# Kernel tuning notes

Hardware: AMD Instinct MI355X
Metric: run time of the kernel (lower is better)

## Reference

```python
import jax, jax.numpy as jnp
import numpy as np

B, S, D = 2, 2048, 2048
H, G = 16, 4
HD = D // H          # head_dim = 128
KV = HD * G          # 512


def setup_inputs() -> dict:
    key = jax.random.key(0)
    ks = jax.random.split(key, 5)
    scale = 1.0 / np.sqrt(D)
    return {
        "x": jax.random.normal(ks[0], (B, S, D), dtype=jnp.float32),
        "Wqkv": jax.random.normal(ks[1], (D, D + 2 * KV), dtype=jnp.float32) * scale,
        "bqkv": jax.random.normal(ks[2], (D + 2 * KV,), dtype=jnp.float32) * 0.01,
        "Wout": jax.random.normal(ks[3], (D, D), dtype=jnp.float32) * scale,
        "bout": jax.random.normal(ks[4], (D,), dtype=jnp.float32) * 0.01,
    }


def reference(x, Wqkv, bqkv, Wout, bout):
    b, s, _ = x.shape
    qkv = x @ Wqkv + bqkv                                  # [b, s, D + 2*KV]
    q, k, v = jnp.split(qkv, [D, D + KV], axis=-1)
    q = q.reshape(b, s, H, HD)                             # [b, s, H, hd]
    # torch .repeat tiles the group axis: head h -> group (h % G)
    k = jnp.tile(k.reshape(b, s, G, HD), (1, 1, H // G, 1))  # [b, s, H, hd]
    v = jnp.tile(v.reshape(b, s, G, HD), (1, 1, H // G, 1))
    # NOTE: original divides by head_dim (not sqrt(head_dim)) -- kept faithfully
    scores = jnp.einsum("bqhd,bkhd->bhqk", q, k) / HD      # [b, H, s, s]
    prob = jax.nn.softmax(scores, axis=-1)
    out = jnp.einsum("bhqk,bkhd->bqhd", prob, v).reshape(b, s, D)
    return out @ Wout + bout
```

## Files before the change

kernel.cpp:

```cpp
#include <hip/hip_runtime.h>
#include <stdint.h>

typedef __bf16 bf16;
typedef __bf16 bf16x8 __attribute__((ext_vector_type(8)));
typedef __bf16 bf16x4 __attribute__((ext_vector_type(4)));
typedef float  f32x4  __attribute__((ext_vector_type(4)));

#define B_   2
#define S_   2048
#define D_   2048
#define H_   16
#define G_   4
#define HD_  128
#define KV_  512
#define NQKV 3072
#define M_   4096

__device__ __forceinline__ void async16(bf16* lds, const bf16* g) {
  __builtin_amdgcn_global_load_lds(
      (const __attribute__((address_space(1))) unsigned int*)g,
      (__attribute__((address_space(3))) unsigned int*)lds, 16, 0, 0);
}

__device__ __forceinline__ f32x4 mfma16(bf16x8 a, bf16x8 b, f32x4 c) {
  return __builtin_amdgcn_mfma_f32_16x16x32_bf16(a, b, c, 0, 0, 0);
}

__global__ void convert_x_kernel(const float* __restrict__ in,
                                 bf16* __restrict__ out, int n4) {
  int i = blockIdx.x * blockDim.x + threadIdx.x;
  if (i >= n4) return;
  float4 v = ((const float4*)in)[i];
  bf16x4 o = { (bf16)v.x, (bf16)v.y, (bf16)v.z, (bf16)v.w };
  *(bf16x4*)(out + (size_t)i * 4) = o;
}

__global__ void transpose_w_kernel(const float* __restrict__ in,
                                   bf16* __restrict__ out,
                                   int rows, int cols) {
  __shared__ float tile[32][33];
  int bc = blockIdx.x * 32;
  int br = blockIdx.y * 32;
  int tx = threadIdx.x, ty = threadIdx.y;
  #pragma unroll
  for (int i = 0; i < 32; i += 8)
    tile[ty + i][tx] = in[(size_t)(br + ty + i) * cols + bc + tx];
  __syncthreads();
  #pragma unroll
  for (int i = 0; i < 32; i += 8)
    out[(size_t)(bc + ty + i) * rows + br + tx] = (bf16)tile[tx][ty + i];
}

__global__ void transpose_v_kernel(const bf16* __restrict__ qkv,
                                   bf16* __restrict__ vt) {
  __shared__ bf16 tile[32][33];
  int bg = blockIdx.z; int b = bg / G_, g = bg % G_;
  int sb = blockIdx.x * 32, db = blockIdx.y * 32;
  int tx = threadIdx.x, ty = threadIdx.y;
  const bf16* src = qkv + (size_t)b * S_ * NQKV + (D_ + KV_ + g * HD_);
  #pragma unroll
  for (int i = 0; i < 32; i += 8)
    tile[ty + i][tx] = src[(size_t)(sb + ty + i) * NQKV + db + tx];
  __syncthreads();
  bf16* dst = vt + (size_t)(b * G_ + g) * HD_ * S_;
  #pragma unroll
  for (int i = 0; i < 32; i += 8)
    dst[(size_t)(db + ty + i) * S_ + sb + tx] = tile[tx][ty + i];
}

template <int OUT_BF16>
__global__ __launch_bounds__(256) void gemm_bt(const bf16* __restrict__ A,
                                               const bf16* __restrict__ Bt,
                                               const float* __restrict__ bias,
                                               void* __restrict__ Cout,
                                               int Ndim, int K) {
  __shared__ __align__(16) bf16 As[128 * 32];
  __shared__ __align__(16) bf16 Bs[128 * 32];
  int t = threadIdx.x;
  int w = t >> 6, l = t & 63, lr = l & 15, lg = l >> 4;
  int wm = w >> 1, wn = w & 1;
  int row0 = blockIdx.x * 128, col0 = blockIdx.y * 128;

  f32x4 acc[4][4] = {};

  const bf16* ga = A  + (size_t)(row0 + (t >> 2)) * K + (t & 3) * 8;
  const bf16* gb = Bt + (size_t)(col0 + (t >> 2)) * K + (t & 3) * 8;

  for (int k0 = 0; k0 < K; k0 += 32) {
    __syncthreads();
    #pragma unroll
    for (int i = 0; i < 2; i++)
      async16(&As[w * 512 + i * 2048], ga + (size_t)i * 64 * K + k0);
    #pragma unroll
    for (int i = 0; i < 2; i++)
      async16(&Bs[w * 512 + i * 2048], gb + (size_t)i * 64 * K + k0);
    __syncthreads();

    bf16x8 af[4], bfr[4];
    #pragma unroll
    for (int mi = 0; mi < 4; mi++)
      af[mi] = *(const bf16x8*)&As[(wm * 64 + mi * 16 + lr) * 32 + lg * 8];
    #pragma unroll
    for (int ni = 0; ni < 4; ni++)
      bfr[ni] = *(const bf16x8*)&Bs[(wn * 64 + ni * 16 + lr) * 32 + lg * 8];
    #pragma unroll
    for (int mi = 0; mi < 4; mi++)
      #pragma unroll
      for (int ni = 0; ni < 4; ni++)
        acc[mi][ni] = mfma16(af[mi], bfr[ni], acc[mi][ni]);
  }

  float bv[4];
  #pragma unroll
  for (int ni = 0; ni < 4; ni++)
    bv[ni] = bias[col0 + wn * 64 + ni * 16 + lr];

  #pragma unroll
  for (int mi = 0; mi < 4; mi++)
    #pragma unroll
    for (int ni = 0; ni < 4; ni++)
      #pragma unroll
      for (int r = 0; r < 4; r++) {
        int row = row0 + wm * 64 + mi * 16 + lg * 4 + r;
        int col = col0 + wn * 64 + ni * 16 + lr;
        float v = acc[mi][ni][r] + bv[ni];
        if (OUT_BF16)
          ((bf16*)Cout)[(size_t)row * Ndim + col] = (bf16)v;
        else
          ((float*)Cout)[(size_t)row * Ndim + col] = v;
      }
}

__global__ __launch_bounds__(256, 2) void attn_kernel(const bf16* __restrict__ qkv,
                                                      const bf16* __restrict__ vt,
                                                      bf16* __restrict__ attnb) {
  __shared__ __align__(16) bf16 Ks[2][64 * 128];
  __shared__ __align__(16) bf16 Vs[2][128 * 64];
  __shared__ __align__(16) bf16 Ps[4][32 * 64];

  int t = threadIdx.x, w = t >> 6, l = t & 63, lr = l & 15, lg = l >> 4;
  int rsw = lr & 7;
  int lin = blockIdx.x + gridDim.x * blockIdx.y;
  int swz = (lin & 7) * 64 + (lin >> 3);
  int q0 = (swz & 15) * 128;
  int bh = swz >> 4, b = bh >> 4, h = bh & 15, g = h & 3;

  bf16x8 qf[2][4];
  #pragma unroll
  for (int mi = 0; mi < 2; mi++) {
    const bf16* qbase = qkv + (size_t)(b * S_ + q0 + w * 32 + mi * 16 + lr) * NQKV + h * HD_;
    #pragma unroll
    for (int kc = 0; kc < 4; kc++)
      qf[mi][kc] = *(const bf16x8*)(qbase + kc * 32 + lg * 8);
  }

  const bf16* kbase = qkv + (size_t)b * S_ * NQKV + D_ + g * HD_;
  const bf16* vbase = vt + (size_t)(b * G_ + g) * HD_ * S_;

  int krowi = w * 4 + (l >> 4);
  int ksw = (l & 15) ^ (krowi & 7);
  const bf16* kgl = kbase + (size_t)krowi * NQKV + ksw * 8;
  int vrowi = w * 8 + (l >> 3);
  int vsw = (l & 7) ^ ((l >> 3) & 7);
  const bf16* vgl = vbase + (size_t)vrowi * S_ + vsw * 8;

  auto STAGE_KV = [&](int nb, int kv0) {
    #pragma unroll
    for (int i = 0; i < 4; i++)
      async16(&Ks[nb][w * 512 + i * 2048], kgl + (size_t)(kv0 + i * 16) * NQKV);
    #pragma unroll
    for (int i = 0; i < 4; i++)
      async16(&Vs[nb][w * 512 + i * 2048], vgl + (size_t)(i * 32) * S_ + kv0);
  };

  float lsump[2] = {};
  f32x4 accO[2][8] = {};

  STAGE_KV(0, 0);

  for (int ti = 0; ti < S_ / 64; ++ti) {
    int cur = ti & 1;
    __syncthreads();
    if (ti + 1 < S_ / 64) STAGE_KV(cur ^ 1, (ti + 1) * 64);

    const bf16* ks = &Ks[cur][0];
    const bf16* vs = &Vs[cur][0];

    f32x4 sacc[2][4] = {};
    __builtin_amdgcn_s_setprio(1);
    #pragma unroll
    for (int fk = 0; fk < 4; fk++) {
      bf16x8 kf[4];
      #pragma unroll
      for (int kc = 0; kc < 4; kc++)
        kf[kc] = *(const bf16x8*)&ks[(fk * 16 + lr) * 128 + (((kc * 4 + lg) ^ rsw) * 8)];
      #pragma unroll
      for (int mi = 0; mi < 2; mi++)
        #pragma unroll
        for (int kc = 0; kc < 4; kc++)
          sacc[mi][fk] = mfma16(kf[kc], qf[mi][kc], sacc[mi][fk]);
    }
    __builtin_amdgcn_s_setprio(0);

    bf16* psw = &Ps[w][0];
    #pragma unroll
    for (int mi = 0; mi < 2; mi++)
      #pragma unroll
      for (int fk = 0; fk < 4; fk++) {
        float p0 = __expf(sacc[mi][fk][0] * 0.0078125f);
        float p1 = __expf(sacc[mi][fk][1] * 0.0078125f);
        float p2 = __expf(sacc[mi][fk][2] * 0.0078125f);
        float p3 = __expf(sacc[mi][fk][3] * 0.0078125f);
        lsump[mi] += (p0 + p1) + (p2 + p3);
        bf16x4 pk = { (bf16)p0, (bf16)p1, (bf16)p2, (bf16)p3 };
        *(bf16x4*)&psw[(mi * 16 + lr) * 64 +
                       (((fk * 2 + (lg >> 1)) ^ rsw) * 8) + (lg & 1) * 4] = pk;
      }

    bf16x8 pa[2][2];
    #pragma unroll
    for (int mi = 0; mi < 2; mi++)
      #pragma unroll
      for (int kk = 0; kk < 2; kk++)
        pa[mi][kk] = *(const bf16x8*)&psw[(mi * 16 + lr) * 64 + (((kk * 4 + lg) ^ rsw) * 8)];

    __builtin_amdgcn_s_setprio(1);
    #pragma unroll
    for (int fd = 0; fd < 8; fd++) {
      bf16x8 vfr[2];
      #pragma unroll
      for (int kk = 0; kk < 2; kk++)
        vfr[kk] = *(const bf16x8*)&vs[(fd * 16 + lr) * 64 + (((kk * 4 + lg) ^ rsw) * 8)];
      #pragma unroll
      for (int mi = 0; mi < 2; mi++)
        #pragma unroll
        for (int kk = 0; kk < 2; kk++)
          accO[mi][fd] = mfma16(pa[mi][kk], vfr[kk], accO[mi][fd]);
    }
    __builtin_amdgcn_s_setprio(0);
  }

  #pragma unroll
  for (int mi = 0; mi < 2; mi++) {
    float s = lsump[mi];
    s += __shfl_xor(s, 16);
    s += __shfl_xor(s, 32);
    float rls[4];
    #pragma unroll
    for (int r = 0; r < 4; r++) rls[r] = 1.f / __shfl(s, lg * 4 + r);
    bf16* obase = attnb + (size_t)(b * S_ + q0 + w * 32 + mi * 16) * D_ + h * HD_;
    #pragma unroll
    for (int r = 0; r < 4; r++)
      #pragma unroll
      for (int fd = 0; fd < 8; fd++)
        obase[(size_t)(lg * 4 + r) * D_ + fd * 16 + lr] =
            (bf16)(accO[mi][fd][r] * rls[r]);
  }
}

extern "C" void kernel_launch(void* const* d_in, const int* in_sizes, int n_in,
                              void* d_out, int out_size, void* d_ws, size_t ws_size,
                              hipStream_t stream) {
  const float* x    = (const float*)d_in[0];
  const float* Wqkv = (const float*)d_in[1];
  const float* bqkv = (const float*)d_in[2];
  const float* Wout = (const float*)d_in[3];
  const float* bout = (const float*)d_in[4];
  float* out = (float*)d_out;

  char* p = (char*)d_ws;
  bf16* xb    = (bf16*)p; p += (size_t)M_ * D_ * 2;
  bf16* wqkvT = (bf16*)p; p += (size_t)NQKV * D_ * 2;
  bf16* woutT = (bf16*)p; p += (size_t)D_ * D_ * 2;
  bf16* qkvb  = (bf16*)p; p += (size_t)M_ * NQKV * 2;
  bf16* vtb   = (bf16*)p; p += (size_t)B_ * G_ * HD_ * S_ * 2;
  bf16* attnb = (bf16*)p; p += (size_t)M_ * D_ * 2;

  convert_x_kernel<<<dim3(M_ * D_ / 4 / 256), dim3(256), 0, stream>>>(x, xb, M_ * D_ / 4);
  transpose_w_kernel<<<dim3(NQKV / 32, D_ / 32), dim3(32, 8), 0, stream>>>(Wqkv, wqkvT, D_, NQKV);
  transpose_w_kernel<<<dim3(D_ / 32, D_ / 32), dim3(32, 8), 0, stream>>>(Wout, woutT, D_, D_);

  gemm_bt<1><<<dim3(M_ / 128, NQKV / 128), dim3(256), 0, stream>>>(xb, wqkvT, bqkv, (void*)qkvb, NQKV, D_);

  transpose_v_kernel<<<dim3(S_ / 32, HD_ / 32, B_ * G_), dim3(32, 8), 0, stream>>>(qkvb, vtb);

  attn_kernel<<<dim3(S_ / 128, B_ * H_), dim3(256), 0, stream>>>(qkvb, vtb, attnb);

  gemm_bt<0><<<dim3(M_ / 128, D_ / 128), dim3(256), 0, stream>>>(attnb, woutT, bout, (void*)out, D_, D_);
}
```

Baseline: 220.1 us.

## Load V fragments directly from global into registers, drop V LDS staging

Removes the V tile from shared memory and loads each wave's V fragments straight from the transposed V buffer in global memory into registers, software-pipelined against the PV MFMAs. It also fuses the exp/softmax step into each QK^T fk chunk so the full sacc array no longer has to be live at once. Launch bounds are raised to 3 waves per SIMD to use the freed LDS and registers. The cost is that V reads now go through global/L2 with per-wave redundancy and exposed latency instead of one shared async copy per block.

```diff
diff --git a/kernel.cpp b/kernel.cpp
--- a/kernel.cpp
+++ b/kernel.cpp
@@ -131,11 +131,10 @@
       }
 }
 
-__global__ __launch_bounds__(256, 2) void attn_kernel(const bf16* __restrict__ qkv,
+__global__ __launch_bounds__(256, 3) void attn_kernel(const bf16* __restrict__ qkv,
                                                       const bf16* __restrict__ vt,
                                                       bf16* __restrict__ attnb) {
   __shared__ __align__(16) bf16 Ks[2][64 * 128];
-  __shared__ __align__(16) bf16 Vs[2][128 * 64];
   __shared__ __align__(16) bf16 Ps[4][32 * 64];
 
   int t = threadIdx.x, w = t >> 6, l = t & 63, lr = l & 15, lg = l >> 4;
@@ -160,33 +159,49 @@
   int krowi = w * 4 + (l >> 4);
   int ksw = (l & 15) ^ (krowi & 7);
   const bf16* kgl = kbase + (size_t)krowi * NQKV + ksw * 8;
-  int vrowi = w * 8 + (l >> 3);
-  int vsw = (l & 7) ^ ((l >> 3) & 7);
-  const bf16* vgl = vbase + (size_t)vrowi * S_ + vsw * 8;
-
-  auto STAGE_KV = [&](int nb, int kv0) {
+  const bf16* vg = vbase + (size_t)lr * S_ + lg * 8;
+
+  auto STAGE_K = [&](int nb, int kv0) {
     #pragma unroll
     for (int i = 0; i < 4; i++)
       async16(&Ks[nb][w * 512 + i * 2048], kgl + (size_t)(kv0 + i * 16) * NQKV);
-    #pragma unroll
-    for (int i = 0; i < 4; i++)
-      async16(&Vs[nb][w * 512 + i * 2048], vgl + (size_t)(i * 32) * S_ + kv0);
   };
+
+#define LOADV(dst, p)                                                         \
+    _Pragma("unroll")                                                         \
+    for (int fd2 = 0; fd2 < 2; fd2++)                                         \
+      _Pragma("unroll")                                                       \
+      for (int kk = 0; kk < 2; kk++)                                          \
+        dst[fd2][kk] = *(const bf16x8*)(vg + (size_t)((p) * 32 + fd2 * 16) * S_ \
+                                        + kv0 + kk * 32);
+
+#define PVQ(p, V)                                                             \
+    _Pragma("unroll")                                                         \
+    for (int fd2 = 0; fd2 < 2; fd2++)                                         \
+      _Pragma("unroll")                                                       \
+      for (int mi = 0; mi < 2; mi++)                                          \
+        _Pragma("unroll")                                                     \
+        for (int kk = 0; kk < 2; kk++)                                        \
+          accO[mi][(p) * 2 + fd2] =                                           \
+              mfma16(pa[mi][kk], V[fd2][kk], accO[mi][(p) * 2 + fd2]);
 
   float lsump[2] = {};
   f32x4 accO[2][8] = {};
 
-  STAGE_KV(0, 0);
+  STAGE_K(0, 0);
 
   for (int ti = 0; ti < S_ / 64; ++ti) {
     int cur = ti & 1;
+    int kv0 = ti * 64;
     __syncthreads();
-    if (ti + 1 < S_ / 64) STAGE_KV(cur ^ 1, (ti + 1) * 64);
+    if (ti + 1 < S_ / 64) STAGE_K(cur ^ 1, kv0 + 64);
+
+    bf16x8 vr0[2][2], vr1[2][2];
+    LOADV(vr0, 0);
 
     const bf16* ks = &Ks[cur][0];
-    const bf16* vs = &Vs[cur][0];
-
-    f32x4 sacc[2][4] = {};
+    bf16* psw = &Ps[w][0];
+
     __builtin_amdgcn_s_setprio(1);
     #pragma unroll
     for (int fk = 0; fk < 4; fk++) {
@@ -194,28 +209,25 @@
       #pragma unroll
       for (int kc = 0; kc < 4; kc++)
         kf[kc] = *(const bf16x8*)&ks[(fk * 16 + lr) * 128 + (((kc * 4 + lg) ^ rsw) * 8)];
+      f32x4 sacc[2] = {};
       #pragma unroll
       for (int mi = 0; mi < 2; mi++)
         #pragma unroll
         for (int kc = 0; kc < 4; kc++)
-          sacc[mi][fk] = mfma16(kf[kc], qf[mi][kc], sacc[mi][fk]);
-    }
-    __builtin_amdgcn_s_setprio(0);
-
-    bf16* psw = &Ps[w][0];
-    #pragma unroll
-    for (int mi = 0; mi < 2; mi++)
-      #pragma unroll
-      for (int fk = 0; fk < 4; fk++) {
-        float p0 = __expf(sacc[mi][fk][0] * 0.0078125f);
-        float p1 = __expf(sacc[mi][fk][1] * 0.0078125f);
-        float p2 = __expf(sacc[mi][fk][2] * 0.0078125f);
-        float p3 = __expf(sacc[mi][fk][3] * 0.0078125f);
+          sacc[mi] = mfma16(kf[kc], qf[mi][kc], sacc[mi]);
+      #pragma unroll
+      for (int mi = 0; mi < 2; mi++) {
+        float p0 = __expf(sacc[mi][0] * 0.0078125f);
+        float p1 = __expf(sacc[mi][1] * 0.0078125f);
+        float p2 = __expf(sacc[mi][2] * 0.0078125f);
+        float p3 = __expf(sacc[mi][3] * 0.0078125f);
         lsump[mi] += (p0 + p1) + (p2 + p3);
         bf16x4 pk = { (bf16)p0, (bf16)p1, (bf16)p2, (bf16)p3 };
         *(bf16x4*)&psw[(mi * 16 + lr) * 64 +
                        (((fk * 2 + (lg >> 1)) ^ rsw) * 8) + (lg & 1) * 4] = pk;
       }
+    }
+    __builtin_amdgcn_s_setprio(0);
 
     bf16x8 pa[2][2];
     #pragma unroll
@@ -225,18 +237,13 @@
         pa[mi][kk] = *(const bf16x8*)&psw[(mi * 16 + lr) * 64 + (((kk * 4 + lg) ^ rsw) * 8)];
 
     __builtin_amdgcn_s_setprio(1);
-    #pragma unroll
-    for (int fd = 0; fd < 8; fd++) {
-      bf16x8 vfr[2];
-      #pragma unroll
-      for (int kk = 0; kk < 2; kk++)
-        vfr[kk] = *(const bf16x8*)&vs[(fd * 16 + lr) * 64 + (((kk * 4 + lg) ^ rsw) * 8)];
-      #pragma unroll
-      for (int mi = 0; mi < 2; mi++)
-        #pragma unroll
-        for (int kk = 0; kk < 2; kk++)
-          accO[mi][fd] = mfma16(pa[mi][kk], vfr[kk], accO[mi][fd]);
-    }
+    LOADV(vr1, 1);
+    PVQ(0, vr0);
+    LOADV(vr0, 2);
+    PVQ(1, vr1);
+    LOADV(vr1, 3);
+    PVQ(2, vr0);
+    PVQ(3, vr1);
     __builtin_amdgcn_s_setprio(0);
   }
 
@@ -256,6 +263,8 @@
         obase[(size_t)(lg * 4 + r) * D_ + fd * 16 + lr] =
             (bf16)(accO[mi][fd][r] * rls[r]);
   }
+#undef LOADV
+#undef PVQ
 }
 
 extern "C" void kernel_launch(void* const* d_in, const int* in_sizes, int n_in,
```

After: 365.8 us. 1.66x slower.

## Halve attention KV tile to 32 and raise occupancy to three blocks per CU

Applied to the files above, without the earlier changes.

Shrinks the per-iteration K/V tile from 64 to 32 keys, halving the LDS footprint of the K, V and P buffers, and raises launch bounds to allow three workgroups per CU. The softmax exponentials are now computed right after each 16-key score fragment, so fewer score accumulators are live at once. The swizzle patterns are adjusted for the narrower tiles. In exchange the loop runs twice as many iterations, each with its own barrier and async staging, so synchronisation overhead grows and there is less MFMA work per barrier to hide latency.

```diff
diff --git a/kernel.cpp b/kernel.cpp
--- a/kernel.cpp
+++ b/kernel.cpp
@@ -131,12 +131,12 @@
       }
 }
 
-__global__ __launch_bounds__(256, 2) void attn_kernel(const bf16* __restrict__ qkv,
+__global__ __launch_bounds__(256, 3) void attn_kernel(const bf16* __restrict__ qkv,
                                                       const bf16* __restrict__ vt,
                                                       bf16* __restrict__ attnb) {
-  __shared__ __align__(16) bf16 Ks[2][64 * 128];
-  __shared__ __align__(16) bf16 Vs[2][128 * 64];
-  __shared__ __align__(16) bf16 Ps[4][32 * 64];
+  __shared__ __align__(16) bf16 Ks[2][32 * 128];
+  __shared__ __align__(16) bf16 Vs[2][128 * 32];
+  __shared__ __align__(16) bf16 Ps[4][32 * 32];
 
   int t = threadIdx.x, w = t >> 6, l = t & 63, lr = l & 15, lg = l >> 4;
   int rsw = lr & 7;
@@ -160,17 +160,17 @@
   int krowi = w * 4 + (l >> 4);
   int ksw = (l & 15) ^ (krowi & 7);
   const bf16* kgl = kbase + (size_t)krowi * NQKV + ksw * 8;
-  int vrowi = w * 8 + (l >> 3);
-  int vsw = (l & 7) ^ ((l >> 3) & 7);
+  int vrowi = w * 16 + (l >> 2);
+  int vsw = (l & 3) ^ (vrowi & 3);
   const bf16* vgl = vbase + (size_t)vrowi * S_ + vsw * 8;
 
   auto STAGE_KV = [&](int nb, int kv0) {
     #pragma unroll
-    for (int i = 0; i < 4; i++)
-      async16(&Ks[nb][w * 512 + i * 2048], kgl + (size_t)(kv0 + i * 16) * NQKV);
-    #pragma unroll
-    for (int i = 0; i < 4; i++)
-      async16(&Vs[nb][w * 512 + i * 2048], vgl + (size_t)(i * 32) * S_ + kv0);
+    for (int i = 0; i < 2; i++)
+      async16(&Ks[nb][i * 2048 + w * 512], kgl + (size_t)(kv0 + i * 16) * NQKV);
+    #pragma unroll
+    for (int i = 0; i < 2; i++)
+      async16(&Vs[nb][i * 2048 + w * 512], vgl + (size_t)(i * 64) * S_ + kv0);
   };
 
   float lsump[2] = {};
@@ -178,64 +178,55 @@
 
   STAGE_KV(0, 0);
 
-  for (int ti = 0; ti < S_ / 64; ++ti) {
+  for (int ti = 0; ti < S_ / 32; ++ti) {
     int cur = ti & 1;
+    int kv0 = ti * 32;
     __syncthreads();
-    if (ti + 1 < S_ / 64) STAGE_KV(cur ^ 1, (ti + 1) * 64);
+    if (ti + 1 < S_ / 32) STAGE_KV(cur ^ 1, kv0 + 32);
 
     const bf16* ks = &Ks[cur][0];
     const bf16* vs = &Vs[cur][0];
-
-    f32x4 sacc[2][4] = {};
+    bf16* psw = &Ps[w][0];
+
     __builtin_amdgcn_s_setprio(1);
     #pragma unroll
-    for (int fk = 0; fk < 4; fk++) {
+    for (int fk = 0; fk < 2; fk++) {
       bf16x8 kf[4];
       #pragma unroll
       for (int kc = 0; kc < 4; kc++)
         kf[kc] = *(const bf16x8*)&ks[(fk * 16 + lr) * 128 + (((kc * 4 + lg) ^ rsw) * 8)];
+      f32x4 sacc[2] = {};
       #pragma unroll
       for (int mi = 0; mi < 2; mi++)
         #pragma unroll
         for (int kc = 0; kc < 4; kc++)
-          sacc[mi][fk] = mfma16(kf[kc], qf[mi][kc], sacc[mi][fk]);
+          sacc[mi] = mfma16(kf[kc], qf[mi][kc], sacc[mi]);
+      #pragma unroll
+      for (int mi = 0; mi < 2; mi++) {
+        float p0 = __expf(sacc[mi][0] * 0.0078125f);
+        float p1 = __expf(sacc[mi][1] * 0.0078125f);
+        float p2 = __expf(sacc[mi][2] * 0.0078125f);
+        float p3 = __expf(sacc[mi][3] * 0.0078125f);
+        lsump[mi] += (p0 + p1) + (p2 + p3);
+        bf16x4 pk = { (bf16)p0, (bf16)p1, (bf16)p2, (bf16)p3 };
+        *(bf16x4*)&psw[(mi * 16 + lr) * 32 +
+                       (((fk * 2 + (lg >> 1)) ^ (lr & 3)) * 8) + (lg & 1) * 4] = pk;
+      }
     }
     __builtin_amdgcn_s_setprio(0);
 
-    bf16* psw = &Ps[w][0];
+    bf16x8 pa[2];
     #pragma unroll
     for (int mi = 0; mi < 2; mi++)
-      #pragma unroll
-      for (int fk = 0; fk < 4; fk++) {
-        float p0 = __expf(sacc[mi][fk][0] * 0.0078125f);
-        float p1 = __expf(sacc[mi][fk][1] * 0.0078125f);
-        float p2 = __expf(sacc[mi][fk][2] * 0.0078125f);
-        float p3 = __expf(sacc[mi][fk][3] * 0.0078125f);
-        lsump[mi] += (p0 + p1) + (p2 + p3);
-        bf16x4 pk = { (bf16)p0, (bf16)p1, (bf16)p2, (bf16)p3 };
-        *(bf16x4*)&psw[(mi * 16 + lr) * 64 +
-                       (((fk * 2 + (lg >> 1)) ^ rsw) * 8) + (lg & 1) * 4] = pk;
-      }
-
-    bf16x8 pa[2][2];
-    #pragma unroll
-    for (int mi = 0; mi < 2; mi++)
-      #pragma unroll
-      for (int kk = 0; kk < 2; kk++)
-        pa[mi][kk] = *(const bf16x8*)&psw[(mi * 16 + lr) * 64 + (((kk * 4 + lg) ^ rsw) * 8)];
+      pa[mi] = *(const bf16x8*)&psw[(mi * 16 + lr) * 32 + ((lg ^ (lr & 3)) * 8)];
 
     __builtin_amdgcn_s_setprio(1);
     #pragma unroll
     for (int fd = 0; fd < 8; fd++) {
-      bf16x8 vfr[2];
-      #pragma unroll
-      for (int kk = 0; kk < 2; kk++)
-        vfr[kk] = *(const bf16x8*)&vs[(fd * 16 + lr) * 64 + (((kk * 4 + lg) ^ rsw) * 8)];
+      bf16x8 vfr = *(const bf16x8*)&vs[(fd * 16 + lr) * 32 + ((lg ^ (lr & 3)) * 8)];
       #pragma unroll
       for (int mi = 0; mi < 2; mi++)
-        #pragma unroll
-        for (int kk = 0; kk < 2; kk++)
-          accO[mi][fd] = mfma16(pa[mi][kk], vfr[kk], accO[mi][fd]);
+        accO[mi][fd] = mfma16(pa[mi], vfr, accO[mi][fd]);
     }
     __builtin_amdgcn_s_setprio(0);
   }
```

Measured after the change: 237.6 us. +8.0%, slower.

## Add 256x256 eight-wave phased GEMM for QKV projection and interleave softmax in attention

Applied to the files above, without the earlier changes.

Adds a new GEMM kernel with 256x256 tiles, 512 threads, and four-phase staggered async loads to LDS, each phase overlapping one slice of the next tile's loads with MFMA work. It replaces the 128x128 GEMM used for the QKV projection. Larger tiles cut global traffic per FLOP, at the cost of more registers and LDS and only 192 blocks in the grid. The attention kernel also computes exp and writes P to LDS per key fragment right after its score MFMAs, which shortens score-register lifetimes and interleaves VALU with MFMA work.

```diff
diff --git a/kernel.cpp b/kernel.cpp
--- a/kernel.cpp
+++ b/kernel.cpp
@@ -131,6 +131,128 @@
       }
 }
 
+template <int OUT_BF16>
+__global__ __launch_bounds__(512, 2) void gemm_8ph(const bf16* __restrict__ A,
+                                                   const bf16* __restrict__ Bt,
+                                                   const float* __restrict__ bias,
+                                                   void* __restrict__ Cout,
+                                                   int Ndim, int K, int nbm) {
+  __shared__ __align__(16) bf16 Ash[2][2][128 * 64];
+  __shared__ __align__(16) bf16 Bsh[2][2][128 * 64];
+
+  int t = threadIdx.x, w = t >> 6, l = t & 63, lr = l & 15, lg = l >> 4;
+  int wm = w >> 2, wn = w & 3;
+  int rsw = lr & 7;
+  int brow0 = (wn & 1) * 64;
+  int bh_ = wn >> 1;
+
+  int cpx = (int)gridDim.x >> 3;
+  int swz = ((int)blockIdx.x & 7) * cpx + ((int)blockIdx.x >> 3);
+  int row0 = (swz % nbm) * 256, col0 = (swz / nbm) * 256;
+
+  int r_ = t >> 3;
+  int csw = (t & 7) ^ (r_ & 7);
+  const bf16* gA = A  + (size_t)(row0 + r_) * K + csw * 8;
+  const bf16* gB = Bt + (size_t)(col0 + r_) * K + csw * 8;
+  int dofs = r_ * 64 + (t & 7) * 8;
+
+  const int NT = K >> 6;
+  f32x4 acc[8][4] = {};
+
+  auto stage2 = [&](int b, int kt, int p) {
+    size_t ko = (size_t)kt * 64;
+    if (p == 0) {
+      async16(&Bsh[b][0][dofs],        gB + ko);
+      async16(&Bsh[b][0][dofs + 4096], gB + (size_t)64 * K + ko);
+    } else if (p == 1) {
+      async16(&Bsh[b][1][dofs],        gB + (size_t)128 * K + ko);
+      async16(&Bsh[b][1][dofs + 4096], gB + (size_t)192 * K + ko);
+    } else if (p == 2) {
+      async16(&Ash[b][0][dofs],        gA + ko);
+      async16(&Ash[b][1][dofs],        gA + (size_t)128 * K + ko);
+    } else {
+      async16(&Ash[b][0][dofs + 4096], gA + (size_t)64 * K + ko);
+      async16(&Ash[b][1][dofs + 4096], gA + (size_t)192 * K + ko);
+    }
+  };
+
+#define LDA8(mi, kc) (*(const bf16x8*)&asb[((mi) * 16 + lr) * 64 + ((((kc) * 4 + lg) ^ rsw) * 8)])
+#define LDB8(ni, kc) (*(const bf16x8*)&bsb[(brow0 + (ni) * 16 + lr) * 64 + ((((kc) * 4 + lg) ^ rsw) * 8)])
+#define PHASE(q) { \
+    bf16x8 a00 = LDA8(2*(q), 0),   a01 = LDA8(2*(q), 1); \
+    bf16x8 a10 = LDA8(2*(q)+1, 0), a11 = LDA8(2*(q)+1, 1); \
+    __builtin_amdgcn_s_setprio(1); \
+    _Pragma("unroll") \
+    for (int ni = 0; ni < 4; ni++) { \
+      acc[2*(q)][ni]   = mfma16(a00, bfr[ni][0], acc[2*(q)][ni]); \
+      acc[2*(q)][ni]   = mfma16(a01, bfr[ni][1], acc[2*(q)][ni]); \
+      acc[2*(q)+1][ni] = mfma16(a10, bfr[ni][0], acc[2*(q)+1][ni]); \
+      acc[2*(q)+1][ni] = mfma16(a11, bfr[ni][1], acc[2*(q)+1][ni]); \
+    } \
+    __builtin_amdgcn_s_setprio(0); }
+
+  stage2(0, 0, 0); stage2(0, 0, 1); stage2(0, 0, 2); stage2(0, 0, 3);
+
+  for (int kt = 0; kt < NT; ++kt) {
+    int bc = kt & 1;
+    int nlast = (kt + 1 < NT);
+    asm volatile("s_waitcnt vmcnt(2)" ::: "memory");
+    __builtin_amdgcn_sched_barrier(0);
+    __builtin_amdgcn_s_barrier();
+
+    const bf16* asb = &Ash[bc][wm][0];
+    const bf16* bsb = &Bsh[bc][bh_][0];
+
+    bf16x8 bfr[4][2];
+    #pragma unroll
+    for (int ni = 0; ni < 4; ni++) {
+      bfr[ni][0] = LDB8(ni, 0);
+      bfr[ni][1] = LDB8(ni, 1);
+    }
+    if (nlast) stage2(bc ^ 1, kt + 1, 0);
+    PHASE(0);
+    __builtin_amdgcn_s_barrier();
+
+    if (nlast) stage2(bc ^ 1, kt + 1, 1);
+    PHASE(1);
+
+    if (nlast) { asm volatile("s_waitcnt vmcnt(4)" ::: "memory"); }
+    else       { asm volatile("s_waitcnt vmcnt(0)" ::: "memory"); }
+    __builtin_amdgcn_sched_barrier(0);
+    __builtin_amdgcn_s_barrier();
+
+    if (nlast) stage2(bc ^ 1, kt + 1, 2);
+    PHASE(2);
+    __builtin_amdgcn_s_barrier();
+
+    if (nlast) stage2(bc ^ 1, kt + 1, 3);
+    PHASE(3);
+  }
+
+  float bv[4];
+  #pragma unroll
+  for (int ni = 0; ni < 4; ni++)
+    bv[ni] = bias[col0 + wn * 64 + ni * 16 + lr];
+
+  #pragma unroll
+  for (int mi = 0; mi < 8; mi++)
+    #pragma unroll
+    for (int ni = 0; ni < 4; ni++)
+      #pragma unroll
+      for (int r = 0; r < 4; r++) {
+        int row = row0 + wm * 128 + mi * 16 + lg * 4 + r;
+        int col = col0 + wn * 64 + ni * 16 + lr;
+        float v = acc[mi][ni][r] + bv[ni];
+        if (OUT_BF16)
+          ((bf16*)Cout)[(size_t)row * Ndim + col] = (bf16)v;
+        else
+          ((float*)Cout)[(size_t)row * Ndim + col] = v;
+      }
+#undef LDA8
+#undef LDB8
+#undef PHASE
+}
+
 __global__ __launch_bounds__(256, 2) void attn_kernel(const bf16* __restrict__ qkv,
                                                       const bf16* __restrict__ vt,
                                                       bf16* __restrict__ attnb) {
@@ -180,13 +302,14 @@
 
   for (int ti = 0; ti < S_ / 64; ++ti) {
     int cur = ti & 1;
+    int kv0 = ti * 64;
     __syncthreads();
-    if (ti + 1 < S_ / 64) STAGE_KV(cur ^ 1, (ti + 1) * 64);
+    if (ti + 1 < S_ / 64) STAGE_KV(cur ^ 1, kv0 + 64);
 
     const bf16* ks = &Ks[cur][0];
     const bf16* vs = &Vs[cur][0];
-
-    f32x4 sacc[2][4] = {};
+    bf16* psw = &Ps[w][0];
+
     __builtin_amdgcn_s_setprio(1);
     #pragma unroll
     for (int fk = 0; fk < 4; fk++) {
@@ -194,28 +317,25 @@
       #pragma unroll
       for (int kc = 0; kc < 4; kc++)
         kf[kc] = *(const bf16x8*)&ks[(fk * 16 + lr) * 128 + (((kc * 4 + lg) ^ rsw) * 8)];
+      f32x4 sacc[2] = {};
       #pragma unroll
       for (int mi = 0; mi < 2; mi++)
         #pragma unroll
         for (int kc = 0; kc < 4; kc++)
-          sacc[mi][fk] = mfma16(kf[kc], qf[mi][kc], sacc[mi][fk]);
-    }
-    __builtin_amdgcn_s_setprio(0);
-
-    bf16* psw = &Ps[w][0];
-    #pragma unroll
-    for (int mi = 0; mi < 2; mi++)
-      #pragma unroll
-      for (int fk = 0; fk < 4; fk++) {
-        float p0 = __expf(sacc[mi][fk][0] * 0.0078125f);
-        float p1 = __expf(sacc[mi][fk][1] * 0.0078125f);
-        float p2 = __expf(sacc[mi][fk][2] * 0.0078125f);
-        float p3 = __expf(sacc[mi][fk][3] * 0.0078125f);
+          sacc[mi] = mfma16(kf[kc], qf[mi][kc], sacc[mi]);
+      #pragma unroll
+      for (int mi = 0; mi < 2; mi++) {
+        float p0 = __expf(sacc[mi][0] * 0.0078125f);
+        float p1 = __expf(sacc[mi][1] * 0.0078125f);
+        float p2 = __expf(sacc[mi][2] * 0.0078125f);
+        float p3 = __expf(sacc[mi][3] * 0.0078125f);
         lsump[mi] += (p0 + p1) + (p2 + p3);
         bf16x4 pk = { (bf16)p0, (bf16)p1, (bf16)p2, (bf16)p3 };
         *(bf16x4*)&psw[(mi * 16 + lr) * 64 +
                        (((fk * 2 + (lg >> 1)) ^ rsw) * 8) + (lg & 1) * 4] = pk;
       }
+    }
+    __builtin_amdgcn_s_setprio(0);
 
     bf16x8 pa[2][2];
     #pragma unroll
@@ -280,7 +400,8 @@
   transpose_w_kernel<<<dim3(NQKV / 32, D_ / 32), dim3(32, 8), 0, stream>>>(Wqkv, wqkvT, D_, NQKV);
   transpose_w_kernel<<<dim3(D_ / 32, D_ / 32), dim3(32, 8), 0, stream>>>(Wout, woutT, D_, D_);
 
-  gemm_bt<1><<<dim3(M_ / 128, NQKV / 128), dim3(256), 0, stream>>>(xb, wqkvT, bqkv, (void*)qkvb, NQKV, D_);
+  gemm_8ph<1><<<dim3((M_ / 256) * (NQKV / 256)), dim3(512), 0, stream>>>(
+      xb, wqkvT, bqkv, (void*)qkvb, NQKV, D_, M_ / 256);
 
   transpose_v_kernel<<<dim3(S_ / 32, HD_ / 32, B_ * G_), dim3(32, 8), 0, stream>>>(qkvb, vtb);
 
```

Measured after the change: 255.1 us. 1.16x slower.
